# Optimization experiments

Hardware: AMD Instinct MI355X
Metric: run time of the kernel (lower is better)

Reference implementation:

```python
import jax, jax.numpy as jnp
import numpy as np

C = 32
H = 8

def _layernorm(x, scale, bias, eps=1e-5):
    mu = jnp.mean(x, axis=-1, keepdims=True)
    var = jnp.mean(jnp.square(x - mu), axis=-1, keepdims=True)
    return (x - mu) * jax.lax.rsqrt(var + eps) * scale + bias


def setup_inputs() -> dict:
    key = jax.random.key(0)
    ks = jax.random.split(key, 10)
    B, s, i, j = 1, 128, 256, 256
    m = jax.random.normal(ks[0], (B, s, i, C), dtype=jnp.float32)
    z = jax.random.normal(ks[1], (B, i, j, C), dtype=jnp.float32)
    sd = 1.0 / np.sqrt(C)
    return {
        "m": m,
        "z": z,
        "ln_scale": jnp.ones((C,), jnp.float32),
        "ln_bias": jnp.zeros((C,), jnp.float32),
        "lnb_scale": jnp.ones((C,), jnp.float32),
        "lnb_bias": jnp.zeros((C,), jnp.float32),
        "wq": jax.random.normal(ks[2], (C, C * H), jnp.float32) * sd,
        "wk": jax.random.normal(ks[3], (C, C * H), jnp.float32) * sd,
        "wv": jax.random.normal(ks[4], (C, C * H), jnp.float32) * sd,
        "wb": jax.random.normal(ks[5], (C, H), jnp.float32) * sd,
        "wg": jax.random.normal(ks[6], (C, C * H), jnp.float32) * sd,
        "wo": jax.random.normal(ks[7], (C * H, C), jnp.float32) * (1.0 / np.sqrt(C * H)),
        "bo": jnp.zeros((C,), jnp.float32),
    }


def reference(m, z, ln_scale, ln_bias, lnb_scale, lnb_bias, wq, wk, wv, wb, wg, wo, bo):
    B, s, i, _ = m.shape
    j = z.shape[2]
    mn = _layernorm(m, ln_scale, ln_bias)                      # (B,s,i,c)
    q = (mn @ wq).reshape(B, s, i, H, C)                        # (B,s,i,h,c)
    k = (mn @ wk).reshape(B, s, i, H, C)
    v = (mn @ wv).reshape(B, s, i, H, C)
    gate = jax.nn.sigmoid(mn @ wg).reshape(B, s, i, H, C)       # (B,s,i,h,c)
    b = (_layernorm(z, lnb_scale, lnb_bias) @ wb)               # (B,i,j,h)
    a = jnp.einsum('bsihc,bsjhc->bsijh', q, k) * (C ** -0.5) + b[:, None]
    a = jax.nn.softmax(a, axis=-2)                              # softmax over j
    o = gate * jnp.einsum('bsijh,bsjhc->bsihc', a, v)
    o = o.reshape(B, s, i, H * C)
    return o @ wo + bo
```

## Files before the change

### kernel.cpp

```cpp
#include <hip/hip_runtime.h>

constexpr int NC = 32;
constexpr int NH = 8;
constexpr int NS = 128;
constexpr int NI = 256;
constexpr int NJ = 256;
constexpr float LN_EPS = 1e-5f;
constexpr float QSCALE = 0.17677669529663687f;
constexpr float LOG2E  = 1.4426950408889634f;

typedef __bf16 bf16x8 __attribute__((ext_vector_type(8)));
typedef __bf16 bf16x2 __attribute__((ext_vector_type(2)));
typedef float floatx4 __attribute__((ext_vector_type(4)));

__device__ __forceinline__ float fexp2(float x) {
#if __has_builtin(__builtin_amdgcn_exp2f)
    return __builtin_amdgcn_exp2f(x);
#else
    return exp2f(x);
#endif
}
__device__ __forceinline__ float frcp(float x) {
#if __has_builtin(__builtin_amdgcn_rcpf)
    return __builtin_amdgcn_rcpf(x);
#else
    return 1.0f / x;
#endif
}
__device__ __forceinline__ unsigned pk2c(float a, float b) {
    union { bf16x2 v; unsigned u; } c;
    c.v = bf16x2{(__bf16)a, (__bf16)b};
    return c.u;
}

__device__ __forceinline__ int qkOff(int row, int chunk) {
    return row * 32 + ((chunk ^ ((row >> 1) & 3)) << 3);
}
__device__ __forceinline__ int vOff(int c, int chunk) {
    return c * 256 + ((chunk ^ (c & 7)) << 3);
}
__device__ __forceinline__ int pOff(int wbase, int row, int chunk) {
    return wbase + row * 32 + ((chunk ^ ((row >> 1) & 3)) << 3);
}

__global__ __launch_bounds__(256) void biasprep_kernel(
    const float* __restrict__ z, const float* __restrict__ lnb_s,
    const float* __restrict__ lnb_b, const float* __restrict__ wb,
    const float* __restrict__ wq, const float* __restrict__ wk,
    const float* __restrict__ wv, const float* __restrict__ wg,
    const float* __restrict__ wo,
    float* __restrict__ bias32, unsigned short* __restrict__ wprep,
    unsigned short* __restrict__ wofrag)
{
    const int b = blockIdx.x;
    const int t = threadIdx.x;
    if (b < 256) {
        __shared__ float zL[256 * 33];
        const float4* src = (const float4*)(z + (size_t)b * NJ * NC);
#pragma unroll
        for (int k = 0; k < 8; ++k) {
            int idx = t + 256 * k;
            float4 v = src[idx];
            int f = idx * 4;
            int j = f >> 5, c = f & 31;
            zL[j * 33 + c]     = v.x; zL[j * 33 + c + 1] = v.y;
            zL[j * 33 + c + 2] = v.z; zL[j * 33 + c + 3] = v.w;
        }
        __syncthreads();

        float x[NC];
#pragma unroll
        for (int c = 0; c < NC; ++c) x[c] = zL[t * 33 + c];
        float mu = 0.f;
#pragma unroll
        for (int c = 0; c < NC; ++c) mu += x[c];
        mu *= (1.0f / NC);
        float var = 0.f;
#pragma unroll
        for (int c = 0; c < NC; ++c) { float d = x[c] - mu; var += d * d; }
        var *= (1.0f / NC);
        float rs = rsqrtf(var + LN_EPS);
        float acc[NH];
#pragma unroll
        for (int h = 0; h < NH; ++h) acc[h] = 0.f;
#pragma unroll
        for (int c = 0; c < NC; ++c) {
            float xn = (x[c] - mu) * rs * lnb_s[c] + lnb_b[c];
#pragma unroll
            for (int h = 0; h < NH; ++h) acc[h] += xn * wb[c * NH + h];
        }
        const int i = b;
        const int w_ = i >> 6, it = (i >> 4) & 3, lm = i & 15;
        const int jc = t >> 5, jt = (t >> 4) & 1, lq = (t >> 2) & 3, r = t & 3;
        const int base = jc * 8192 + w_ * 2048 + (jt * 4 + it) * 256
                       + (lq * 16 + lm) * 4 + r;
#pragma unroll
        for (int h = 0; h < NH; ++h)
            bias32[h * 65536 + base] = acc[h] * LOG2E;
    } else if (b < 272) {
        int g = (b - 256) * 256 + t;
        int p  = g >> 10;
        int h  = (g >> 7) & 7;
        int ct = (g >> 6) & 1;
        int l  = g & 63;
        const float* W = (p == 0) ? wq : (p == 1) ? wk : (p == 2) ? wv : wg;
        float scale = (p == 0) ? QSCALE * LOG2E : (p == 3) ? LOG2E : 1.0f;
        int col = 32 * h + 16 * ct + (l & 15);
        int r0  = 8 * (l >> 4);
        float v[8];
#pragma unroll
        for (int e = 0; e < 8; ++e) v[e] = W[(r0 + e) * 256 + col] * scale;
        uint4 u;
        u.x = pk2c(v[0], v[1]); u.y = pk2c(v[2], v[3]);
        u.z = pk2c(v[4], v[5]); u.w = pk2c(v[6], v[7]);
        *(uint4*)&wprep[g * 8] = u;
    } else {
        int g = (b - 272) * 256 + t;
        int tile = g >> 6;
        int l = g & 63;
        int kt = tile >> 1, nt = tile & 1;
        int r0 = kt * 32 + 8 * (l >> 4);
        int col = nt * 16 + (l & 15);
        float v[8];
#pragma unroll
        for (int e = 0; e < 8; ++e) v[e] = wo[(r0 + e) * 32 + col];
        uint4 u;
        u.x = pk2c(v[0], v[1]); u.y = pk2c(v[2], v[3]);
        u.z = pk2c(v[4], v[5]); u.w = pk2c(v[6], v[7]);
        *(uint4*)&wofrag[g * 8] = u;
    }
}

__global__ __launch_bounds__(256, 4) void attn_kernel(
    const float* __restrict__ m, const float* __restrict__ ln_s,
    const float* __restrict__ ln_b,
    const unsigned short* __restrict__ wprep,
    const float* __restrict__ bias32,
    unsigned short* __restrict__ attn16)
{
    __shared__ unsigned short KX[256 * 32];
    __shared__ unsigned short Vt[32 * 256];
    __shared__ unsigned short Pbuf[4 * 512];

    const int t = threadIdx.x;
    const int h = blockIdx.x & 7;
    const int s = blockIdx.x >> 3;
    const int l = t & 63, w = t >> 6;
    const int lm = l & 15, lq = l >> 4;
    const int ibase = w * 64;
    const int pwb = w * 512;
    const floatx4 zero = {0.f, 0.f, 0.f, 0.f};

    {
        const float4* mr = (const float4*)(m + ((size_t)s * NI + t) * NC);
        float x[NC];
#pragma unroll
        for (int k = 0; k < 8; ++k) {
            float4 v = mr[k];
            x[4*k] = v.x; x[4*k+1] = v.y; x[4*k+2] = v.z; x[4*k+3] = v.w;
        }
        float mu = 0.f;
#pragma unroll
        for (int c = 0; c < NC; ++c) mu += x[c];
        mu *= (1.0f / NC);
        float var = 0.f;
#pragma unroll
        for (int c = 0; c < NC; ++c) { float d = x[c] - mu; var += d * d; }
        var *= (1.0f / NC);
        float rs = rsqrtf(var + LN_EPS);
#pragma unroll
        for (int k = 0; k < 4; ++k) {
            uint4 u;
            u.x = pk2c((x[8*k+0]-mu)*rs*ln_s[8*k+0]+ln_b[8*k+0],
                       (x[8*k+1]-mu)*rs*ln_s[8*k+1]+ln_b[8*k+1]);
            u.y = pk2c((x[8*k+2]-mu)*rs*ln_s[8*k+2]+ln_b[8*k+2],
                       (x[8*k+3]-mu)*rs*ln_s[8*k+3]+ln_b[8*k+3]);
            u.z = pk2c((x[8*k+4]-mu)*rs*ln_s[8*k+4]+ln_b[8*k+4],
                       (x[8*k+5]-mu)*rs*ln_s[8*k+5]+ln_b[8*k+5]);
            u.w = pk2c((x[8*k+6]-mu)*rs*ln_s[8*k+6]+ln_b[8*k+6],
                       (x[8*k+7]-mu)*rs*ln_s[8*k+7]+ln_b[8*k+7]);
            *(uint4*)&KX[qkOff(t, k)] = u;
        }
    }

    const unsigned short* wp = wprep + ((size_t)h * 128 + l) * 8;
    bf16x8 wfQ[2], wfK[2], wfV[2];
#pragma unroll
    for (int ct = 0; ct < 2; ++ct) {
        wfQ[ct] = *(const bf16x8*)&wp[(0 * 1024 + ct * 64) * 8];
        wfK[ct] = *(const bf16x8*)&wp[(1 * 1024 + ct * 64) * 8];
        wfV[ct] = *(const bf16x8*)&wp[(2 * 1024 + ct * 64) * 8];
    }
    bf16x8 Xb[4];
#pragma unroll
    for (int it = 0; it < 4; ++it)
        Xb[it] = *(const bf16x8*)&KX[qkOff(ibase + it * 16 + lm, lq)];

#pragma unroll
    for (int it = 0; it < 4; ++it)
#pragma unroll
        for (int ct = 0; ct < 2; ++ct) {
            floatx4 d = __builtin_amdgcn_mfma_f32_16x16x32_bf16(wfQ[ct], Xb[it], zero, 0, 0, 0);
            uint2 u; u.x = pk2c(d[0], d[1]); u.y = pk2c(d[2], d[3]);
            int row = ibase + it * 16 + lm;
            *(uint2*)&KX[qkOff(row, 2 * ct + (lq >> 1)) + (lq & 1) * 4] = u;
        }
    bf16x8 Qb[4];
#pragma unroll
    for (int it = 0; it < 4; ++it)
        Qb[it] = *(const bf16x8*)&KX[qkOff(ibase + it * 16 + lm, lq)];

#pragma unroll
    for (int it = 0; it < 4; ++it)
#pragma unroll
        for (int ct = 0; ct < 2; ++ct) {
            floatx4 d = __builtin_amdgcn_mfma_f32_16x16x32_bf16(wfK[ct], Xb[it], zero, 0, 0, 0);
            uint2 u; u.x = pk2c(d[0], d[1]); u.y = pk2c(d[2], d[3]);
            int row = ibase + it * 16 + lm;
            *(uint2*)&KX[qkOff(row, 2 * ct + (lq >> 1)) + (lq & 1) * 4] = u;
        }

#pragma unroll
    for (int jt = 0; jt < 4; ++jt)
#pragma unroll
        for (int ct = 0; ct < 2; ++ct) {
            floatx4 d = __builtin_amdgcn_mfma_f32_16x16x32_bf16(Xb[jt], wfV[ct], zero, 0, 0, 0);
            uint2 u; u.x = pk2c(d[0], d[1]); u.y = pk2c(d[2], d[3]);
            int c = ct * 16 + lm;
            int chunk = 8 * w + 2 * jt + (lq >> 1);
            *(uint2*)&Vt[vOff(c, chunk) + (lq & 1) * 4] = u;
        }

    __syncthreads();

    floatx4 accO[2][4];
#pragma unroll
    for (int ct = 0; ct < 2; ++ct)
#pragma unroll
        for (int it = 0; it < 4; ++it) accO[ct][it] = zero;
    float accLv[4] = {0.f, 0.f, 0.f, 0.f};

    const float* bptr = bias32 + (size_t)h * 65536 + w * 2048 + l * 4;

    for (int jc = 0; jc < 8; ++jc) {
        const float* bj = bptr + jc * 8192;
        bf16x8 Ka0 = *(const bf16x8*)&KX[qkOff(jc * 32 + lm, lq)];
        bf16x8 Ka1 = *(const bf16x8*)&KX[qkOff(jc * 32 + 16 + lm, lq)];
        bf16x8 Va0 = *(const bf16x8*)&Vt[vOff(lm, 4 * jc + lq)];
        bf16x8 Va1 = *(const bf16x8*)&Vt[vOff(16 + lm, 4 * jc + lq)];
#pragma unroll
        for (int it = 0; it < 4; ++it) {
            floatx4 C0 = *(const floatx4*)(bj + it * 256);
            floatx4 S0 = __builtin_amdgcn_mfma_f32_16x16x32_bf16(Ka0, Qb[it], C0, 0, 0, 0);
            floatx4 C1 = *(const floatx4*)(bj + (4 + it) * 256);
            floatx4 S1 = __builtin_amdgcn_mfma_f32_16x16x32_bf16(Ka1, Qb[it], C1, 0, 0, 0);
            float p0 = fexp2(S0[0]), p1 = fexp2(S0[1]);
            float p2 = fexp2(S0[2]), p3 = fexp2(S0[3]);
            float p4 = fexp2(S1[0]), p5 = fexp2(S1[1]);
            float p6 = fexp2(S1[2]), p7 = fexp2(S1[3]);
            accLv[it] += ((p0 + p1) + (p2 + p3)) + ((p4 + p5) + (p6 + p7));
            uint2 u0; u0.x = pk2c(p0, p1); u0.y = pk2c(p2, p3);
            uint2 u1; u1.x = pk2c(p4, p5); u1.y = pk2c(p6, p7);
            *(uint2*)&Pbuf[pOff(pwb, lm, 0 + (lq >> 1)) + (lq & 1) * 4] = u0;
            *(uint2*)&Pbuf[pOff(pwb, lm, 2 + (lq >> 1)) + (lq & 1) * 4] = u1;
            bf16x8 Pb = *(const bf16x8*)&Pbuf[pOff(pwb, lm, lq)];
            accO[0][it] = __builtin_amdgcn_mfma_f32_16x16x32_bf16(Va0, Pb, accO[0][it], 0, 0, 0);
            accO[1][it] = __builtin_amdgcn_mfma_f32_16x16x32_bf16(Va1, Pb, accO[1][it], 0, 0, 0);
        }
    }

    {
        bf16x8 wfG0 = *(const bf16x8*)&wp[(3 * 1024 + 0 * 64) * 8];
        bf16x8 wfG1 = *(const bf16x8*)&wp[(3 * 1024 + 1 * 64) * 8];
#pragma unroll
        for (int it = 0; it < 4; ++it) {
            float L = accLv[it];
            L += __shfl_xor(L, 16, 64);
            L += __shfl_xor(L, 32, 64);
            const float inv = frcp(L);
            floatx4 d0 = __builtin_amdgcn_mfma_f32_16x16x32_bf16(wfG0, Xb[it], zero, 0, 0, 0);
            floatx4 d1 = __builtin_amdgcn_mfma_f32_16x16x32_bf16(wfG1, Xb[it], zero, 0, 0, 0);
            const size_t rowb = ((size_t)s * NI + ibase + it * 16 + lm) * 256 + h * 32;
            {
                float o0 = accO[0][it][0] * inv * frcp(1.0f + fexp2(-d0[0]));
                float o1 = accO[0][it][1] * inv * frcp(1.0f + fexp2(-d0[1]));
                float o2 = accO[0][it][2] * inv * frcp(1.0f + fexp2(-d0[2]));
                float o3 = accO[0][it][3] * inv * frcp(1.0f + fexp2(-d0[3]));
                uint2 u; u.x = pk2c(o0, o1); u.y = pk2c(o2, o3);
                *(uint2*)&attn16[rowb + 0 * 16 + lq * 4] = u;
            }
            {
                float o0 = accO[1][it][0] * inv * frcp(1.0f + fexp2(-d1[0]));
                float o1 = accO[1][it][1] * inv * frcp(1.0f + fexp2(-d1[1]));
                float o2 = accO[1][it][2] * inv * frcp(1.0f + fexp2(-d1[2]));
                float o3 = accO[1][it][3] * inv * frcp(1.0f + fexp2(-d1[3]));
                uint2 u; u.x = pk2c(o0, o1); u.y = pk2c(o2, o3);
                *(uint2*)&attn16[rowb + 1 * 16 + lq * 4] = u;
            }
        }
    }
}

__global__ __launch_bounds__(256) void proj_kernel(
    const unsigned short* __restrict__ attn16,
    const unsigned short* __restrict__ wofrag,
    const float* __restrict__ bo, float* __restrict__ out)
{
    const int t = threadIdx.x;
    const int l = t & 63, w = t >> 6;
    const int lm = l & 15, lq = l >> 4;
    const int row0 = blockIdx.x * 128 + w * 32;
    const floatx4 zero = {0.f, 0.f, 0.f, 0.f};

    floatx4 acc[2][2];
#pragma unroll
    for (int it = 0; it < 2; ++it)
#pragma unroll
        for (int nt = 0; nt < 2; ++nt) acc[it][nt] = zero;

#pragma unroll 2
    for (int kt = 0; kt < 8; ++kt) {
        bf16x8 a0 = *(const bf16x8*)&attn16[(size_t)(row0 + lm) * 256 + kt * 32 + lq * 8];
        bf16x8 a1 = *(const bf16x8*)&attn16[(size_t)(row0 + 16 + lm) * 256 + kt * 32 + lq * 8];
        bf16x8 b0 = *(const bf16x8*)&wofrag[((kt * 2 + 0) * 64 + l) * 8];
        bf16x8 b1 = *(const bf16x8*)&wofrag[((kt * 2 + 1) * 64 + l) * 8];
        acc[0][0] = __builtin_amdgcn_mfma_f32_16x16x32_bf16(a0, b0, acc[0][0], 0, 0, 0);
        acc[0][1] = __builtin_amdgcn_mfma_f32_16x16x32_bf16(a0, b1, acc[0][1], 0, 0, 0);
        acc[1][0] = __builtin_amdgcn_mfma_f32_16x16x32_bf16(a1, b0, acc[1][0], 0, 0, 0);
        acc[1][1] = __builtin_amdgcn_mfma_f32_16x16x32_bf16(a1, b1, acc[1][1], 0, 0, 0);
    }

    float bov[2] = {bo[lm], bo[16 + lm]};
#pragma unroll
    for (int it = 0; it < 2; ++it)
#pragma unroll
        for (int nt = 0; nt < 2; ++nt)
#pragma unroll
            for (int r = 0; r < 4; ++r)
                out[(size_t)(row0 + it * 16 + lq * 4 + r) * NC + nt * 16 + lm]
                    = acc[it][nt][r] + bov[nt];
}

extern "C" void kernel_launch(void* const* d_in, const int* in_sizes, int n_in,
                              void* d_out, int out_size, void* d_ws, size_t ws_size,
                              hipStream_t stream) {
    const float* m     = (const float*)d_in[0];
    const float* z     = (const float*)d_in[1];
    const float* ln_s  = (const float*)d_in[2];
    const float* ln_b  = (const float*)d_in[3];
    const float* lnb_s = (const float*)d_in[4];
    const float* lnb_b = (const float*)d_in[5];
    const float* wq    = (const float*)d_in[6];
    const float* wk    = (const float*)d_in[7];
    const float* wv    = (const float*)d_in[8];
    const float* wb    = (const float*)d_in[9];
    const float* wg    = (const float*)d_in[10];
    const float* wo    = (const float*)d_in[11];
    const float* bo    = (const float*)d_in[12];
    float* out = (float*)d_out;

    float* bias32 = (float*)d_ws;
    unsigned short* wprep  = (unsigned short*)((char*)d_ws + (2u << 20));
    unsigned short* wofrag = (unsigned short*)((char*)d_ws + (2u << 20) + 65536);
    unsigned short* attn16 = (unsigned short*)((char*)d_ws + (2u << 20) + 65536 + 16384);

    biasprep_kernel<<<276, 256, 0, stream>>>(z, lnb_s, lnb_b, wb, wq, wk, wv, wg,
                                             wo, bias32, wprep, wofrag);
    attn_kernel<<<NS * NH, 256, 0, stream>>>(m, ln_s, ln_b, wprep, bias32, attn16);
    proj_kernel<<<(NS * NI) / 128, 256, 0, stream>>>(attn16, wofrag, bo, out);
}
```

Before: 123.6 us.

## Fuse attention and output projection into one kernel looping over heads

Merges the attention and projection kernels. Each block now handles one sequence row and a quarter of the i positions, loops over all 8 heads, and accumulates the output projection in registers, so the bf16 intermediate is no longer written to and read back from global memory. In exchange, K and V for every head are recomputed per i-quarter, which is four times the K/V projection work. The grid also drops to 512 blocks with extra syncthreads per head, which lowers parallelism and occupancy.

```diff
diff --git a/kernel.cpp b/kernel.cpp
--- a/kernel.cpp
+++ b/kernel.cpp
@@ -131,23 +131,23 @@
     }
 }
 
-__global__ __launch_bounds__(256, 4) void attn_kernel(
+__global__ __launch_bounds__(256, 2) void mega_kernel(
     const float* __restrict__ m, const float* __restrict__ ln_s,
     const float* __restrict__ ln_b,
     const unsigned short* __restrict__ wprep,
     const float* __restrict__ bias32,
-    unsigned short* __restrict__ attn16)
+    const unsigned short* __restrict__ wofrag,
+    const float* __restrict__ bo, float* __restrict__ out)
 {
     __shared__ unsigned short KX[256 * 32];
     __shared__ unsigned short Vt[32 * 256];
     __shared__ unsigned short Pbuf[4 * 512];
 
     const int t = threadIdx.x;
-    const int h = blockIdx.x & 7;
-    const int s = blockIdx.x >> 3;
+    const int s  = blockIdx.x >> 2;
+    const int iq = blockIdx.x & 3;
     const int l = t & 63, w = t >> 6;
     const int lm = l & 15, lq = l >> 4;
-    const int ibase = w * 64;
     const int pwb = w * 512;
     const floatx4 zero = {0.f, 0.f, 0.f, 0.f};
 
@@ -182,163 +182,122 @@
             *(uint4*)&KX[qkOff(t, k)] = u;
         }
     }
-
-    const unsigned short* wp = wprep + ((size_t)h * 128 + l) * 8;
-    bf16x8 wfQ[2], wfK[2], wfV[2];
-#pragma unroll
-    for (int ct = 0; ct < 2; ++ct) {
-        wfQ[ct] = *(const bf16x8*)&wp[(0 * 1024 + ct * 64) * 8];
-        wfK[ct] = *(const bf16x8*)&wp[(1 * 1024 + ct * 64) * 8];
-        wfV[ct] = *(const bf16x8*)&wp[(2 * 1024 + ct * 64) * 8];
-    }
-    bf16x8 Xb[4];
+    __syncthreads();
+
+    bf16x8 Xb4[4];
 #pragma unroll
     for (int it = 0; it < 4; ++it)
-        Xb[it] = *(const bf16x8*)&KX[qkOff(ibase + it * 16 + lm, lq)];
-
-#pragma unroll
-    for (int it = 0; it < 4; ++it)
+        Xb4[it] = *(const bf16x8*)&KX[qkOff(w * 64 + it * 16 + lm, lq)];
+    bf16x8 Xq = *(const bf16x8*)&KX[qkOff(iq * 64 + w * 16 + lm, lq)];
+
+    floatx4 accP[2] = {zero, zero};
+
+    for (int h = 0; h < NH; ++h) {
+        const unsigned short* wp = wprep + ((size_t)h * 128 + l) * 8;
+        bf16x8 wfQ[2], wfK[2], wfV[2];
 #pragma unroll
         for (int ct = 0; ct < 2; ++ct) {
-            floatx4 d = __builtin_amdgcn_mfma_f32_16x16x32_bf16(wfQ[ct], Xb[it], zero, 0, 0, 0);
+            wfQ[ct] = *(const bf16x8*)&wp[(0 * 1024 + ct * 64) * 8];
+            wfK[ct] = *(const bf16x8*)&wp[(1 * 1024 + ct * 64) * 8];
+            wfV[ct] = *(const bf16x8*)&wp[(2 * 1024 + ct * 64) * 8];
+        }
+        __syncthreads();
+
+#pragma unroll
+        for (int it = 0; it < 4; ++it)
+#pragma unroll
+            for (int ct = 0; ct < 2; ++ct) {
+                floatx4 d = __builtin_amdgcn_mfma_f32_16x16x32_bf16(wfK[ct], Xb4[it], zero, 0, 0, 0);
+                uint2 u; u.x = pk2c(d[0], d[1]); u.y = pk2c(d[2], d[3]);
+                int row = w * 64 + it * 16 + lm;
+                *(uint2*)&KX[qkOff(row, 2 * ct + (lq >> 1)) + (lq & 1) * 4] = u;
+            }
+#pragma unroll
+        for (int jt = 0; jt < 4; ++jt)
+#pragma unroll
+            for (int ct = 0; ct < 2; ++ct) {
+                floatx4 d = __builtin_amdgcn_mfma_f32_16x16x32_bf16(Xb4[jt], wfV[ct], zero, 0, 0, 0);
+                uint2 u; u.x = pk2c(d[0], d[1]); u.y = pk2c(d[2], d[3]);
+                int c = ct * 16 + lm;
+                int chunk = 8 * w + 2 * jt + (lq >> 1);
+                *(uint2*)&Vt[vOff(c, chunk) + (lq & 1) * 4] = u;
+            }
+#pragma unroll
+        for (int ct = 0; ct < 2; ++ct) {
+            floatx4 d = __builtin_amdgcn_mfma_f32_16x16x32_bf16(wfQ[ct], Xq, zero, 0, 0, 0);
             uint2 u; u.x = pk2c(d[0], d[1]); u.y = pk2c(d[2], d[3]);
-            int row = ibase + it * 16 + lm;
-            *(uint2*)&KX[qkOff(row, 2 * ct + (lq >> 1)) + (lq & 1) * 4] = u;
-        }
-    bf16x8 Qb[4];
-#pragma unroll
-    for (int it = 0; it < 4; ++it)
-        Qb[it] = *(const bf16x8*)&KX[qkOff(ibase + it * 16 + lm, lq)];
-
-#pragma unroll
-    for (int it = 0; it < 4; ++it)
-#pragma unroll
-        for (int ct = 0; ct < 2; ++ct) {
-            floatx4 d = __builtin_amdgcn_mfma_f32_16x16x32_bf16(wfK[ct], Xb[it], zero, 0, 0, 0);
-            uint2 u; u.x = pk2c(d[0], d[1]); u.y = pk2c(d[2], d[3]);
-            int row = ibase + it * 16 + lm;
-            *(uint2*)&KX[qkOff(row, 2 * ct + (lq >> 1)) + (lq & 1) * 4] = u;
-        }
-
-#pragma unroll
-    for (int jt = 0; jt < 4; ++jt)
-#pragma unroll
-        for (int ct = 0; ct < 2; ++ct) {
-            floatx4 d = __builtin_amdgcn_mfma_f32_16x16x32_bf16(Xb[jt], wfV[ct], zero, 0, 0, 0);
-            uint2 u; u.x = pk2c(d[0], d[1]); u.y = pk2c(d[2], d[3]);
-            int c = ct * 16 + lm;
-            int chunk = 8 * w + 2 * jt + (lq >> 1);
-            *(uint2*)&Vt[vOff(c, chunk) + (lq & 1) * 4] = u;
-        }
-
-    __syncthreads();
-
-    floatx4 accO[2][4];
-#pragma unroll
-    for (int ct = 0; ct < 2; ++ct)
-#pragma unroll
-        for (int it = 0; it < 4; ++it) accO[ct][it] = zero;
-    float accLv[4] = {0.f, 0.f, 0.f, 0.f};
-
-    const float* bptr = bias32 + (size_t)h * 65536 + w * 2048 + l * 4;
-
-    for (int jc = 0; jc < 8; ++jc) {
-        const float* bj = bptr + jc * 8192;
-        bf16x8 Ka0 = *(const bf16x8*)&KX[qkOff(jc * 32 + lm, lq)];
-        bf16x8 Ka1 = *(const bf16x8*)&KX[qkOff(jc * 32 + 16 + lm, lq)];
-        bf16x8 Va0 = *(const bf16x8*)&Vt[vOff(lm, 4 * jc + lq)];
-        bf16x8 Va1 = *(const bf16x8*)&Vt[vOff(16 + lm, 4 * jc + lq)];
-#pragma unroll
-        for (int it = 0; it < 4; ++it) {
-            floatx4 C0 = *(const floatx4*)(bj + it * 256);
-            floatx4 S0 = __builtin_amdgcn_mfma_f32_16x16x32_bf16(Ka0, Qb[it], C0, 0, 0, 0);
-            floatx4 C1 = *(const floatx4*)(bj + (4 + it) * 256);
-            floatx4 S1 = __builtin_amdgcn_mfma_f32_16x16x32_bf16(Ka1, Qb[it], C1, 0, 0, 0);
+            *(uint2*)&Pbuf[pOff(pwb, lm, 2 * ct + (lq >> 1)) + (lq & 1) * 4] = u;
+        }
+        bf16x8 Qb = *(const bf16x8*)&Pbuf[pOff(pwb, lm, lq)];
+
+        __syncthreads();
+
+        float accLv = 0.f;
+        floatx4 accO0 = zero, accO1 = zero;
+        const float* bj0 = bias32 + (size_t)h * 65536 + iq * 2048 + w * 256 + l * 4;
+
+        for (int jc = 0; jc < 8; ++jc) {
+            const float* bj = bj0 + jc * 8192;
+            bf16x8 Ka0 = *(const bf16x8*)&KX[qkOff(jc * 32 + lm, lq)];
+            bf16x8 Ka1 = *(const bf16x8*)&KX[qkOff(jc * 32 + 16 + lm, lq)];
+            bf16x8 Va0 = *(const bf16x8*)&Vt[vOff(lm, 4 * jc + lq)];
+            bf16x8 Va1 = *(const bf16x8*)&Vt[vOff(16 + lm, 4 * jc + lq)];
+            floatx4 C0 = *(const floatx4*)(bj);
+            floatx4 S0 = __builtin_amdgcn_mfma_f32_16x16x32_bf16(Ka0, Qb, C0, 0, 0, 0);
+            floatx4 C1 = *(const floatx4*)(bj + 1024);
+            floatx4 S1 = __builtin_amdgcn_mfma_f32_16x16x32_bf16(Ka1, Qb, C1, 0, 0, 0);
             float p0 = fexp2(S0[0]), p1 = fexp2(S0[1]);
             float p2 = fexp2(S0[2]), p3 = fexp2(S0[3]);
             float p4 = fexp2(S1[0]), p5 = fexp2(S1[1]);
             float p6 = fexp2(S1[2]), p7 = fexp2(S1[3]);
-            accLv[it] += ((p0 + p1) + (p2 + p3)) + ((p4 + p5) + (p6 + p7));
+            accLv += ((p0 + p1) + (p2 + p3)) + ((p4 + p5) + (p6 + p7));
             uint2 u0; u0.x = pk2c(p0, p1); u0.y = pk2c(p2, p3);
             uint2 u1; u1.x = pk2c(p4, p5); u1.y = pk2c(p6, p7);
             *(uint2*)&Pbuf[pOff(pwb, lm, 0 + (lq >> 1)) + (lq & 1) * 4] = u0;
             *(uint2*)&Pbuf[pOff(pwb, lm, 2 + (lq >> 1)) + (lq & 1) * 4] = u1;
             bf16x8 Pb = *(const bf16x8*)&Pbuf[pOff(pwb, lm, lq)];
-            accO[0][it] = __builtin_amdgcn_mfma_f32_16x16x32_bf16(Va0, Pb, accO[0][it], 0, 0, 0);
-            accO[1][it] = __builtin_amdgcn_mfma_f32_16x16x32_bf16(Va1, Pb, accO[1][it], 0, 0, 0);
-        }
-    }
-
-    {
-        bf16x8 wfG0 = *(const bf16x8*)&wp[(3 * 1024 + 0 * 64) * 8];
-        bf16x8 wfG1 = *(const bf16x8*)&wp[(3 * 1024 + 1 * 64) * 8];
-#pragma unroll
-        for (int it = 0; it < 4; ++it) {
-            float L = accLv[it];
+            accO0 = __builtin_amdgcn_mfma_f32_16x16x32_bf16(Va0, Pb, accO0, 0, 0, 0);
+            accO1 = __builtin_amdgcn_mfma_f32_16x16x32_bf16(Va1, Pb, accO1, 0, 0, 0);
+        }
+
+        {
+            float L = accLv;
             L += __shfl_xor(L, 16, 64);
             L += __shfl_xor(L, 32, 64);
             const float inv = frcp(L);
-            floatx4 d0 = __builtin_amdgcn_mfma_f32_16x16x32_bf16(wfG0, Xb[it], zero, 0, 0, 0);
-            floatx4 d1 = __builtin_amdgcn_mfma_f32_16x16x32_bf16(wfG1, Xb[it], zero, 0, 0, 0);
-            const size_t rowb = ((size_t)s * NI + ibase + it * 16 + lm) * 256 + h * 32;
-            {
-                float o0 = accO[0][it][0] * inv * frcp(1.0f + fexp2(-d0[0]));
-                float o1 = accO[0][it][1] * inv * frcp(1.0f + fexp2(-d0[1]));
-                float o2 = accO[0][it][2] * inv * frcp(1.0f + fexp2(-d0[2]));
-                float o3 = accO[0][it][3] * inv * frcp(1.0f + fexp2(-d0[3]));
-                uint2 u; u.x = pk2c(o0, o1); u.y = pk2c(o2, o3);
-                *(uint2*)&attn16[rowb + 0 * 16 + lq * 4] = u;
-            }
-            {
-                float o0 = accO[1][it][0] * inv * frcp(1.0f + fexp2(-d1[0]));
-                float o1 = accO[1][it][1] * inv * frcp(1.0f + fexp2(-d1[1]));
-                float o2 = accO[1][it][2] * inv * frcp(1.0f + fexp2(-d1[2]));
-                float o3 = accO[1][it][3] * inv * frcp(1.0f + fexp2(-d1[3]));
-                uint2 u; u.x = pk2c(o0, o1); u.y = pk2c(o2, o3);
-                *(uint2*)&attn16[rowb + 1 * 16 + lq * 4] = u;
-            }
+            bf16x8 wfG0 = *(const bf16x8*)&wp[(3 * 1024 + 0 * 64) * 8];
+            bf16x8 wfG1 = *(const bf16x8*)&wp[(3 * 1024 + 1 * 64) * 8];
+            floatx4 g0 = __builtin_amdgcn_mfma_f32_16x16x32_bf16(wfG0, Xq, zero, 0, 0, 0);
+            floatx4 g1 = __builtin_amdgcn_mfma_f32_16x16x32_bf16(wfG1, Xq, zero, 0, 0, 0);
+            float o0 = accO0[0] * inv * frcp(1.0f + fexp2(-g0[0]));
+            float o1 = accO0[1] * inv * frcp(1.0f + fexp2(-g0[1]));
+            float o2 = accO0[2] * inv * frcp(1.0f + fexp2(-g0[2]));
+            float o3 = accO0[3] * inv * frcp(1.0f + fexp2(-g0[3]));
+            float o4 = accO1[0] * inv * frcp(1.0f + fexp2(-g1[0]));
+            float o5 = accO1[1] * inv * frcp(1.0f + fexp2(-g1[1]));
+            float o6 = accO1[2] * inv * frcp(1.0f + fexp2(-g1[2]));
+            float o7 = accO1[3] * inv * frcp(1.0f + fexp2(-g1[3]));
+            uint2 u0; u0.x = pk2c(o0, o1); u0.y = pk2c(o2, o3);
+            uint2 u1; u1.x = pk2c(o4, o5); u1.y = pk2c(o6, o7);
+            *(uint2*)&Pbuf[pOff(pwb, lm, 0 + (lq >> 1)) + (lq & 1) * 4] = u0;
+            *(uint2*)&Pbuf[pOff(pwb, lm, 2 + (lq >> 1)) + (lq & 1) * 4] = u1;
+            bf16x8 of = *(const bf16x8*)&Pbuf[pOff(pwb, lm, lq)];
+            bf16x8 wob0 = *(const bf16x8*)&wofrag[((size_t)(h * 2 + 0) * 64 + l) * 8];
+            bf16x8 wob1 = *(const bf16x8*)&wofrag[((size_t)(h * 2 + 1) * 64 + l) * 8];
+            accP[0] = __builtin_amdgcn_mfma_f32_16x16x32_bf16(of, wob0, accP[0], 0, 0, 0);
+            accP[1] = __builtin_amdgcn_mfma_f32_16x16x32_bf16(of, wob1, accP[1], 0, 0, 0);
         }
     }
-}
-
-__global__ __launch_bounds__(256) void proj_kernel(
-    const unsigned short* __restrict__ attn16,
-    const unsigned short* __restrict__ wofrag,
-    const float* __restrict__ bo, float* __restrict__ out)
-{
-    const int t = threadIdx.x;
-    const int l = t & 63, w = t >> 6;
-    const int lm = l & 15, lq = l >> 4;
-    const int row0 = blockIdx.x * 128 + w * 32;
-    const floatx4 zero = {0.f, 0.f, 0.f, 0.f};
-
-    floatx4 acc[2][2];
-#pragma unroll
-    for (int it = 0; it < 2; ++it)
-#pragma unroll
-        for (int nt = 0; nt < 2; ++nt) acc[it][nt] = zero;
-
-#pragma unroll 2
-    for (int kt = 0; kt < 8; ++kt) {
-        bf16x8 a0 = *(const bf16x8*)&attn16[(size_t)(row0 + lm) * 256 + kt * 32 + lq * 8];
-        bf16x8 a1 = *(const bf16x8*)&attn16[(size_t)(row0 + 16 + lm) * 256 + kt * 32 + lq * 8];
-        bf16x8 b0 = *(const bf16x8*)&wofrag[((kt * 2 + 0) * 64 + l) * 8];
-        bf16x8 b1 = *(const bf16x8*)&wofrag[((kt * 2 + 1) * 64 + l) * 8];
-        acc[0][0] = __builtin_amdgcn_mfma_f32_16x16x32_bf16(a0, b0, acc[0][0], 0, 0, 0);
-        acc[0][1] = __builtin_amdgcn_mfma_f32_16x16x32_bf16(a0, b1, acc[0][1], 0, 0, 0);
-        acc[1][0] = __builtin_amdgcn_mfma_f32_16x16x32_bf16(a1, b0, acc[1][0], 0, 0, 0);
-        acc[1][1] = __builtin_amdgcn_mfma_f32_16x16x32_bf16(a1, b1, acc[1][1], 0, 0, 0);
+
+    {
+        float bov0 = bo[lm], bov1 = bo[16 + lm];
+        const size_t row0 = (size_t)s * NI + iq * 64 + w * 16 + lq * 4;
+#pragma unroll
+        for (int r = 0; r < 4; ++r) {
+            out[(row0 + r) * NC + lm]      = accP[0][r] + bov0;
+            out[(row0 + r) * NC + 16 + lm] = accP[1][r] + bov1;
+        }
     }
-
-    float bov[2] = {bo[lm], bo[16 + lm]};
-#pragma unroll
-    for (int it = 0; it < 2; ++it)
-#pragma unroll
-        for (int nt = 0; nt < 2; ++nt)
-#pragma unroll
-            for (int r = 0; r < 4; ++r)
-                out[(size_t)(row0 + it * 16 + lq * 4 + r) * NC + nt * 16 + lm]
-                    = acc[it][nt][r] + bov[nt];
 }
 
 extern "C" void kernel_launch(void* const* d_in, const int* in_sizes, int n_in,
@@ -362,10 +321,9 @@
     float* bias32 = (float*)d_ws;
     unsigned short* wprep  = (unsigned short*)((char*)d_ws + (2u << 20));
     unsigned short* wofrag = (unsigned short*)((char*)d_ws + (2u << 20) + 65536);
-    unsigned short* attn16 = (unsigned short*)((char*)d_ws + (2u << 20) + 65536 + 16384);
 
     biasprep_kernel<<<276, 256, 0, stream>>>(z, lnb_s, lnb_b, wb, wq, wk, wv, wg,
                                              wo, bias32, wprep, wofrag);
-    attn_kernel<<<NS * NH, 256, 0, stream>>>(m, ln_s, ln_b, wprep, bias32, attn16);
-    proj_kernel<<<(NS * NI) / 128, 256, 0, stream>>>(attn16, wofrag, bo, out);
-}
+    mega_kernel<<<NS * 4, 256, 0, stream>>>(m, ln_s, ln_b, wprep, bias32,
+                                            wofrag, bo, out);
+}
```

New measurement: 150.1 us. +21.4%, slower.
